# Performance work log

Measured on AMD Instinct MI355X. Metric: run time of the kernel, lower is better.

The kernel has to match this reference:

```python
import jax, jax.numpy as jnp
import numpy as np

N = 1024          # nodes per atom and per input graph / barycenter
K = 8             # num_atoms
OT_LAYERS = 3     # proximal-point outer iterations inside fgwd
SINKHORN_LAYERS = 3
GWB_LAYERS = 2    # barycenter alternating-optimization iterations
PROX_BETA = 0.1   # proximal / entropic regularization strength
EPS = 1e-16


def fgwd(Gs, ps, Gb, pb):
    """Gromov-Wasserstein distance via proximal point + Sinkhorn.
    Gs:(ns,ns), ps:(ns,1), Gb:(nb,nb), pb:(nb,1). Returns (d, T) with T:(ns,nb).
    Square-loss GW cost: c(T) = f1(Gs) ps 1^T + 1 (f2(Gb) pb)^T - 2 Gs T Gb^T."""
    ns, nb = Gs.shape[0], Gb.shape[0]
    cost_st = ((Gs * Gs) @ ps) + ((Gb * Gb) @ pb).T  # (ns,1)+(1,nb) -> (ns,nb)
    T0 = ps @ pb.T  # independent-coupling init

    def ot_step(T, _):
        cost = cost_st - 2.0 * (Gs @ T @ Gb.T)
        kernel = jnp.exp(-cost / PROX_BETA) * T  # proximal-point kernel

        def sink(carry, _):
            a, b = carry
            b = pb / (kernel.T @ a + EPS)
            a = ps / (kernel @ b + EPS)
            return (a, b), None

        (a, b), _ = jax.lax.scan(sink, (ps, pb), None, length=SINKHORN_LAYERS)
        return (a * kernel) * b.T, None

    T, _ = jax.lax.scan(ot_step, T0, None, length=OT_LAYERS)
    cost = cost_st - 2.0 * (Gs @ T @ Gb.T)
    d = jnp.sum(cost * T)
    return d, T


def setup_inputs() -> dict:
    key = jax.random.key(0)
    k1, k2, k3 = jax.random.split(key, 3)
    Gm = jax.random.uniform(k1, (N, N), jnp.float32)          # input graph (sigmoid-range adjacency)
    pm = jnp.ones((N, 1), jnp.float32) / N                    # uniform node distribution
    atoms_presig = jax.random.normal(k2, (K, N, N), jnp.float32)  # pre-sigmoid atom params
    probs = jnp.ones((K, N, 1), jnp.float32) / N              # uniform atom distributions
    weights = jax.nn.softmax(jax.random.normal(k3, (K,), jnp.float32))  # output_weights
    return {"Gm": Gm, "pm": pm, "atoms_presig": atoms_presig, "probs": probs,
            "weights": weights}


def reference(Gm, pm, atoms_presig, probs, weights):
    Gk = jax.nn.sigmoid(atoms_presig)              # output_atoms: (K,N,N)
    G_bary, pb = Gm, pm                            # init_mode=0 -> barycenter init from input M
    fgwd_v = jax.vmap(fgwd, in_axes=(0, 0, None, None))
    denom = pb @ pb.T                              # pb pb^T normalizer
    for _ in range(GWB_LAYERS):
        _, trans = fgwd_v(Gk, probs, G_bary, pb)   # trans: (K,N,N)
        # comp_fgwb: sum_k w_k * T_k^T G_k T_k / (pb pb^T)
        GT = jnp.einsum('knm,kmj->knj', Gk, trans)
        G_bary = jnp.einsum('k,kni,knj->ij', weights, trans, GT) / denom
    d_fgw, _ = fgwd(Gm, pm, G_bary, pb)
    return d_fgw, G_bary
```

## Files before the change

### kernel.cpp

```cpp
#include <hip/hip_runtime.h>
#include <math.h>

#define N_   1024
#define K_   8
#define OTL  3
#define SKL  3
#define GWBL 2
#define INVB 10.0f
#define EPSV 1e-16f
#define INVN (1.0f / 1024.0f)
#define NN   ((size_t)N_ * N_)

typedef __attribute__((ext_vector_type(8))) short short8;
typedef __attribute__((ext_vector_type(4))) float f32x4;
typedef unsigned short bfu;

__device__ __forceinline__ float b2f(bfu u) {
    unsigned x = ((unsigned)u) << 16;
    return __builtin_bit_cast(float, x);
}
__device__ __forceinline__ bfu f2b(float f) {
    unsigned u = __builtin_bit_cast(unsigned, f);
    unsigned r = u + 0x7fffu + ((u >> 16) & 1u);
    return (bfu)(r >> 16);
}

template<int EPI>
__global__ __launch_bounds__(256, 2)
void bgemm_k(const bfu* __restrict__ A, const bfu* __restrict__ B,
             void* __restrict__ Cp, size_t sA, size_t sB, size_t sC,
             const float* __restrict__ rv, const float* __restrict__ cv,
             const float* __restrict__ wts, float* __restrict__ rs) {
    __shared__ bfu As[128 * 32];
    __shared__ bfu Bs[128 * 32];

    const int z  = blockIdx.x;
    const int bm = blockIdx.y * 128, bn = blockIdx.z * 128;
    const int tid = threadIdx.x;
    const int lane = tid & 63, wv = tid >> 6;
    const int wr = wv >> 1, wc = wv & 1;

    if (EPI == 0) {
        if (rs && blockIdx.y == 0 && blockIdx.z == 0) {
            float4 zf = {0.f, 0.f, 0.f, 0.f};
            *(float4*)&rs[z * N_ + tid * 4] = zf;
        }
    }

    const bfu* Az = A + (size_t)z * sA;
    const bfu* Bz = B + (size_t)z * sB;

    const int sr = tid >> 2;
    const int sk = (tid & 3) * 8;
    const int fr = lane & 15;
    const int ks = (lane >> 4) * 8;

    f32x4 acc[4][4];
    #pragma unroll
    for (int i = 0; i < 4; i++)
        #pragma unroll
        for (int j = 0; j < 4; j++) acc[i][j] = (f32x4)0.f;

    for (int k0 = 0; k0 < N_; k0 += 32) {
        __syncthreads();
        #pragma unroll
        for (int h = 0; h < 2; ++h) {
            const int row = sr + h * 64;
            const bfu* ga = Az + (size_t)(bm + row) * N_ + k0 + sk;
            const bfu* gb = Bz + (size_t)(bn + row) * N_ + k0 + sk;
            __builtin_amdgcn_global_load_lds(
                (const __attribute__((address_space(1))) unsigned int*)ga,
                (__attribute__((address_space(3))) unsigned int*)&As[row * 32 + sk],
                16, 0, 0);
            __builtin_amdgcn_global_load_lds(
                (const __attribute__((address_space(1))) unsigned int*)gb,
                (__attribute__((address_space(3))) unsigned int*)&Bs[row * 32 + sk],
                16, 0, 0);
        }
        __syncthreads();

        short8 af[4], bf[4];
        #pragma unroll
        for (int mi = 0; mi < 4; ++mi)
            af[mi] = *(const short8*)&As[(wr * 64 + mi * 16 + fr) * 32 + ks];
        #pragma unroll
        for (int ni = 0; ni < 4; ++ni)
            bf[ni] = *(const short8*)&Bs[(wc * 64 + ni * 16 + fr) * 32 + ks];
        #pragma unroll
        for (int mi = 0; mi < 4; ++mi)
            #pragma unroll
            for (int ni = 0; ni < 4; ++ni)
                acc[mi][ni] = __builtin_amdgcn_mfma_f32_16x16x32_bf16(
                    af[mi], bf[ni], acc[mi][ni], 0, 0, 0);
    }

    const int r0 = bm + wr * 64, c0 = bn + wc * 64;
    const int rq = (lane >> 4) * 4;

    if (EPI == 1) {
        float* Cz = (float*)Cp + (size_t)z * sC;
        const float w = wts[z];
        #pragma unroll
        for (int mi = 0; mi < 4; ++mi)
            #pragma unroll
            for (int ni = 0; ni < 4; ++ni)
                #pragma unroll
                for (int q = 0; q < 4; ++q)
                    Cz[(size_t)(r0 + mi * 16 + rq + q) * N_ + c0 + ni * 16 + fr]
                        = w * acc[mi][ni][q];
    } else if (EPI == 0) {
        bfu* Cz = (bfu*)Cp + (size_t)z * sC;
        #pragma unroll
        for (int mi = 0; mi < 4; ++mi)
            #pragma unroll
            for (int ni = 0; ni < 4; ++ni)
                #pragma unroll
                for (int q = 0; q < 4; ++q)
                    Cz[(size_t)(r0 + mi * 16 + rq + q) * N_ + c0 + ni * 16 + fr]
                        = f2b(acc[mi][ni][q]);
    } else {
        bfu* Cz = (bfu*)Cp + (size_t)z * sC;
        const float* rvz = rv + z * N_;
        float rsum[4][4];
        #pragma unroll
        for (int mi = 0; mi < 4; ++mi)
            #pragma unroll
            for (int q = 0; q < 4; ++q) rsum[mi][q] = 0.f;
        #pragma unroll
        for (int mi = 0; mi < 4; ++mi)
            #pragma unroll
            for (int ni = 0; ni < 4; ++ni)
                #pragma unroll
                for (int q = 0; q < 4; ++q) {
                    const int row = r0 + mi * 16 + rq + q;
                    const int col = c0 + ni * 16 + fr;
                    const float cost = rvz[col] + cv[row] - 2.f * acc[mi][ni][q];
                    const float t = b2f(Cz[(size_t)row * N_ + col]);
                    const bfu tn = f2b(expf(-cost * INVB) * t);
                    Cz[(size_t)row * N_ + col] = tn;
                    rsum[mi][q] += b2f(tn);
                }
        #pragma unroll
        for (int mi = 0; mi < 4; ++mi)
            #pragma unroll
            for (int q = 0; q < 4; ++q) {
                float v = rsum[mi][q];
                v += __shfl_xor(v, 1);
                v += __shfl_xor(v, 2);
                v += __shfl_xor(v, 4);
                v += __shfl_xor(v, 8);
                if (fr == 0)
                    atomicAdd(&rs[z * N_ + r0 + mi * 16 + rq + q], v);
            }
    }
}

template<int EPI>
__global__ __launch_bounds__(256, 2)
void gemm64_k(const bfu* __restrict__ A, const bfu* __restrict__ B,
              void* __restrict__ Cp,
              const float* __restrict__ rv, const float* __restrict__ cv,
              float* __restrict__ rs, float* __restrict__ dout) {
    __shared__ bfu As[64 * 32];
    __shared__ bfu Bs[64 * 32];
    const int bn = blockIdx.x * 64;
    const int bm = blockIdx.y * 64;
    const int tid = threadIdx.x;
    const int lane = tid & 63, wv = tid >> 6;
    const int wr = wv >> 1, wc = wv & 1;
    const int sr = tid >> 2, sk = (tid & 3) * 8;
    const int fr = lane & 15, ks = (lane >> 4) * 8;

    if (EPI == 0) {
        if (blockIdx.x == 0 && blockIdx.y == 0) {
            if (rs) {
                float4 zf = {0.f, 0.f, 0.f, 0.f};
                *(float4*)&rs[tid * 4] = zf;
            }
            if (dout && tid == 0) *dout = 0.f;
        }
    }

    f32x4 acc[2][2];
    #pragma unroll
    for (int i = 0; i < 2; i++)
        #pragma unroll
        for (int j = 0; j < 2; j++) acc[i][j] = (f32x4)0.f;

    for (int k0 = 0; k0 < N_; k0 += 32) {
        __syncthreads();
        __builtin_amdgcn_global_load_lds(
            (const __attribute__((address_space(1))) unsigned int*)
                (A + (size_t)(bm + sr) * N_ + k0 + sk),
            (__attribute__((address_space(3))) unsigned int*)&As[sr * 32 + sk],
            16, 0, 0);
        __builtin_amdgcn_global_load_lds(
            (const __attribute__((address_space(1))) unsigned int*)
                (B + (size_t)(bn + sr) * N_ + k0 + sk),
            (__attribute__((address_space(3))) unsigned int*)&Bs[sr * 32 + sk],
            16, 0, 0);
        __syncthreads();
        short8 af[2], bf[2];
        #pragma unroll
        for (int mi = 0; mi < 2; ++mi)
            af[mi] = *(const short8*)&As[(wr * 32 + mi * 16 + fr) * 32 + ks];
        #pragma unroll
        for (int ni = 0; ni < 2; ++ni)
            bf[ni] = *(const short8*)&Bs[(wc * 32 + ni * 16 + fr) * 32 + ks];
        #pragma unroll
        for (int mi = 0; mi < 2; ++mi)
            #pragma unroll
            for (int ni = 0; ni < 2; ++ni)
                acc[mi][ni] = __builtin_amdgcn_mfma_f32_16x16x32_bf16(
                    af[mi], bf[ni], acc[mi][ni], 0, 0, 0);
    }

    const int r0 = bm + wr * 32, c0 = bn + wc * 32;
    const int rq = (lane >> 4) * 4;

    if (EPI == 0) {
        bfu* C = (bfu*)Cp;
        #pragma unroll
        for (int mi = 0; mi < 2; ++mi)
            #pragma unroll
            for (int ni = 0; ni < 2; ++ni)
                #pragma unroll
                for (int q = 0; q < 4; ++q)
                    C[(size_t)(r0 + mi * 16 + rq + q) * N_ + c0 + ni * 16 + fr]
                        = f2b(acc[mi][ni][q]);
    } else if (EPI == 2) {
        bfu* C = (bfu*)Cp;
        float rsum[2][4];
        #pragma unroll
        for (int mi = 0; mi < 2; ++mi)
            #pragma unroll
            for (int q = 0; q < 4; ++q) rsum[mi][q] = 0.f;
        #pragma unroll
        for (int mi = 0; mi < 2; ++mi)
            #pragma unroll
            for (int ni = 0; ni < 2; ++ni)
                #pragma unroll
                for (int q = 0; q < 4; ++q) {
                    const int row = r0 + mi * 16 + rq + q;
                    const int col = c0 + ni * 16 + fr;
                    const float cost = rv[col] + cv[row] - 2.f * acc[mi][ni][q];
                    const float t = b2f(C[(size_t)row * N_ + col]);
                    const bfu tn = f2b(expf(-cost * INVB) * t);
                    C[(size_t)row * N_ + col] = tn;
                    rsum[mi][q] += b2f(tn);
                }
        #pragma unroll
        for (int mi = 0; mi < 2; ++mi)
            #pragma unroll
            for (int q = 0; q < 4; ++q) {
                float v = rsum[mi][q];
                v += __shfl_xor(v, 1);
                v += __shfl_xor(v, 2);
                v += __shfl_xor(v, 4);
                v += __shfl_xor(v, 8);
                if (fr == 0)
                    atomicAdd(&rs[r0 + mi * 16 + rq + q], v);
            }
    } else {
        const bfu* C = (const bfu*)Cp;
        float bs = 0.f;
        #pragma unroll
        for (int mi = 0; mi < 2; ++mi)
            #pragma unroll
            for (int ni = 0; ni < 2; ++ni)
                #pragma unroll
                for (int q = 0; q < 4; ++q) {
                    const int row = r0 + mi * 16 + rq + q;
                    const int col = c0 + ni * 16 + fr;
                    bs += (rv[col] + cv[row] - 2.f * acc[mi][ni][q]) *
                          b2f(C[(size_t)row * N_ + col]);
                }
        #pragma unroll
        for (int off = 32; off; off >>= 1) bs += __shfl_down(bs, off);
        __shared__ float wred[4];
        if (lane == 0) wred[wv] = bs;
        __syncthreads();
        if (tid == 0) atomicAdd(dout, wred[0] + wred[1] + wred[2] + wred[3]);
    }
}

__global__ __launch_bounds__(256)
void prox1_k(bfu* __restrict__ Tt, const float* __restrict__ c2,
             const float* __restrict__ u, const float* __restrict__ d2,
             const float* __restrict__ w, const float* __restrict__ ps,
             const float* __restrict__ pb, float* __restrict__ bv,
             int zs, int nb) {
    const int b = blockIdx.x;
    const int z  = (nb == 8) ? (b & 7) : 0;
    const int rp = (nb == 8) ? (b >> 3) : b;
    const int tid = threadIdx.x;
    const int half = tid >> 7;
    const int j = rp * 2 + half;
    const int i0 = (tid & 127) * 8;
    const float d2j = d2[j], wj = w[j], pbj = pb[j];
    const float* c2z = c2 + z * zs + i0;
    const float* uz  = u  + z * zs + i0;
    const float* psz = ps + z * zs + i0;
    bfu o[8];
    float s = 0.f;
    #pragma unroll
    for (int t = 0; t < 8; ++t) {
        const float cost = c2z[t] + d2j - 2.f * uz[t] * wj;
        o[t] = f2b(expf(-cost * INVB) * psz[t] * pbj);
        s += b2f(o[t]);
    }
    *(short8*)&Tt[((size_t)z << 20) + ((size_t)j << 10) + i0] = *(short8*)o;
    #pragma unroll
    for (int off = 32; off; off >>= 1) s += __shfl_down(s, off);
    __shared__ float red[4];
    if ((tid & 63) == 0) red[tid >> 6] = s;
    __syncthreads();
    if ((tid & 127) == 0)
        bv[z * N_ + j] = pbj / ((red[half * 2] + red[half * 2 + 1]) * INVN + EPSV);
}


__global__ void sinkb_k(const bfu* __restrict__ Tt, const float* __restrict__ a0,
                        const float* __restrict__ pb, float* __restrict__ bv) {
    int z, jb;
    if (gridDim.y == 8) { z = blockIdx.x & 7; jb = (blockIdx.x >> 3) + (blockIdx.y << 5); }
    else                { z = 0;              jb = blockIdx.x; }
    const int wv = threadIdx.x >> 6, lane = threadIdx.x & 63;
    const int j = jb * 4 + wv;
    const bfu* Tr = Tt + (size_t)z * NN + (size_t)j * N_;
    const float* az = a0 + z * N_;
    float s = 0.f;
    for (int c = lane * 8; c < N_; c += 512) {
        bfu t[8];
        *(short8*)t = *(const short8*)&Tr[c];
        #pragma unroll
        for (int q = 0; q < 8; ++q) s += b2f(t[q]) * az[c + q];
    }
    #pragma unroll
    for (int off = 32; off; off >>= 1) s += __shfl_down(s, off);
    if (lane == 0) bv[z * N_ + j] = pb[j] / (s + EPSV);
}

template<int NB, int RS, int TUPD>
__global__ __launch_bounds__(1024)
void sinka_k(bfu* __restrict__ Tt, const float* __restrict__ bvin,
             const float* __restrict__ rs, const float* __restrict__ ps, int pstr,
             float* __restrict__ av) {
    constexpr int CPB = (NB == 8) ? 32 : 16;
    constexpr int RG  = 1024 / CPB;
    constexpr int RPG = N_ / RG;
    int z, cb;
    if (NB == 8) { z = blockIdx.x & 7; cb = blockIdx.x >> 3; }
    else         { z = 0;              cb = blockIdx.x; }
    const int tid = threadIdx.x;
    const int cl = tid % CPB, rg = tid / CPB;
    const int i = cb * CPB + cl;
    bfu* Tz = Tt + (size_t)z * NN;

    __shared__ float bvs[1024];
    __shared__ float red[1024];
    if (RS) bvs[tid] = INVN / (rs[z * N_ + tid] * INVN + EPSV);
    else    bvs[tid] = bvin[z * N_ + tid];
    __syncthreads();

    float s = 0.f;
    const int j0 = rg * RPG;
    #pragma unroll 8
    for (int j = j0; j < j0 + RPG; ++j)
        s += b2f(Tz[(size_t)j * N_ + i]) * bvs[j];
    red[tid] = s;
    __syncthreads();
    #pragma unroll
    for (int h = RG / 2; h > 0; h >>= 1) {
        if (rg < h) red[rg * CPB + cl] += red[(rg + h) * CPB + cl];
        __syncthreads();
    }
    const float avi = ps[z * pstr + i] / (red[cl] + EPSV);
    if (!TUPD) {
        if (rg == 0) av[z * N_ + i] = avi;
    } else {
        for (int j = j0; j < j0 + RPG; ++j) {
            const size_t o = (size_t)j * N_ + i;
            Tz[o] = f2b(b2f(Tz[o]) * avi * bvs[j]);
        }
    }
}


template<int SIG>
__global__ void prep_k(const float* __restrict__ X, bfu* __restrict__ Y,
                       float* __restrict__ y2, float* __restrict__ y1) {
    const int z = blockIdx.y;
    const int wv = threadIdx.x >> 6, lane = threadIdx.x & 63;
    const int r = blockIdx.x * 4 + wv;
    const float* Xr = X + (size_t)z * NN + (size_t)r * N_;
    bfu* Yr = Y + (size_t)z * NN + (size_t)r * N_;
    float s2 = 0.f, s1 = 0.f;
    for (int c = lane * 4; c < N_; c += 256) {
        float4 v = *(const float4*)(Xr + c);
        if (SIG) {
            v.x = 1.f / (1.f + expf(-v.x));
            v.y = 1.f / (1.f + expf(-v.y));
            v.z = 1.f / (1.f + expf(-v.z));
            v.w = 1.f / (1.f + expf(-v.w));
        }
        bfu o[4];
        o[0] = f2b(v.x); o[1] = f2b(v.y); o[2] = f2b(v.z); o[3] = f2b(v.w);
        *(ulong1*)&Yr[c] = *(ulong1*)o;
        s2 += v.x * v.x + v.y * v.y + v.z * v.z + v.w * v.w;
        s1 += v.x + v.y + v.z + v.w;
    }
    #pragma unroll
    for (int off = 32; off; off >>= 1) {
        s2 += __shfl_down(s2, off);
        s1 += __shfl_down(s1, off);
    }
    if (lane == 0) {
        y2[z * N_ + r] = s2 * INVN;
        y1[z * N_ + r] = s1 * INVN;
    }
}

__global__ void reduce8_k(const float* __restrict__ part, bfu* __restrict__ Gbt,
                          float* __restrict__ d2, float* __restrict__ w,
                          float* __restrict__ out1) {
    const int tid = threadIdx.x;
    __shared__ float wred[8];
    #pragma unroll
    for (int rep = 0; rep < 2; ++rep) {
        const int row = blockIdx.x + rep * 512;
        const size_t idx = (size_t)row * N_ + tid * 4;
        float4 s = *(const float4*)(part + idx);
        #pragma unroll
        for (int sl = 1; sl < K_; ++sl) {
            float4 v = *(const float4*)(part + (size_t)sl * NN + idx);
            s.x += v.x; s.y += v.y; s.z += v.z; s.w += v.w;
        }
        const float sc = 1048576.f;
        s.x *= sc; s.y *= sc; s.z *= sc; s.w *= sc;
        bfu o[4];
        o[0] = f2b(s.x); o[1] = f2b(s.y); o[2] = f2b(s.z); o[3] = f2b(s.w);
        *(ulong1*)&Gbt[idx] = *(ulong1*)o;
        if (out1) {
            out1[idx + 0] = s.x; out1[idx + 1] = s.y;
            out1[idx + 2] = s.z; out1[idx + 3] = s.w;
        }
        float r2 = s.x * s.x + s.y * s.y + s.z * s.z + s.w * s.w;
        float r1 = s.x + s.y + s.z + s.w;
        #pragma unroll
        for (int off = 32; off; off >>= 1) {
            r2 += __shfl_down(r2, off);
            r1 += __shfl_down(r1, off);
        }
        if ((tid & 63) == 0) {
            wred[(tid >> 6) * 2]     = r2;
            wred[(tid >> 6) * 2 + 1] = r1;
        }
        __syncthreads();
        if (tid == 0) {
            d2[row] = (wred[0] + wred[2] + wred[4] + wred[6]) * INVN;
            w[row]  = (wred[1] + wred[3] + wred[5] + wred[7]) * INVN;
        }
        __syncthreads();
    }
}


template<int NB, int RS1>
static inline void sink_tail(bfu* Tt, const float* ps, int pstr, const float* pm,
                             float* avec, float* bvec, float* rs, hipStream_t stream) {
    const dim3 ga((NB == 8) ? 256 : 64);
    const dim3 gb(256, NB);
    const dim3 blk(256);
    sinka_k<NB, RS1, 0><<<ga, dim3(1024), 0, stream>>>(Tt, bvec, rs, ps, pstr, avec);
    sinkb_k<<<gb, blk, 0, stream>>>(Tt, avec, pm, bvec);
    sinka_k<NB, 0, 0><<<ga, dim3(1024), 0, stream>>>(Tt, bvec, rs, ps, pstr, avec);
    sinkb_k<<<gb, blk, 0, stream>>>(Tt, avec, pm, bvec);
    sinka_k<NB, 0, 1><<<ga, dim3(1024), 0, stream>>>(Tt, bvec, rs, ps, pstr, avec);
}

extern "C" void kernel_launch(void* const* d_in, const int* in_sizes, int n_in,
                              void* d_out, int out_size, void* d_ws, size_t ws_size,
                              hipStream_t stream) {
    const float* Gm    = (const float*)d_in[0];
    const float* pm    = (const float*)d_in[1];
    const float* atoms = (const float*)d_in[2];
    const float* probs = (const float*)d_in[3];
    const float* wts   = (const float*)d_in[4];
    float* out = (float*)d_out;

    char* base = (char*)d_ws;
    bfu*   Gkt  = (bfu*)base;                    base += K_ * NN * 2;
    bfu*   Tt   = (bfu*)base;                    base += K_ * NN * 2;
    bfu*   M    = (bfu*)base;                    base += K_ * NN * 2;
    float* part = (float*)base;                  base += K_ * NN * 4;
    bfu*   Gbt  = (bfu*)base;                    base += NN * 2;
    bfu*   Gmt  = (bfu*)base;                    base += NN * 2;
    float* Gk2ps = (float*)base;                 base += K_ * N_ * 4;
    float* Gku   = (float*)base;                 base += K_ * N_ * 4;
    float* Gm2pm = (float*)base;                 base += N_ * 4;
    float* Gmu   = (float*)base;                 base += N_ * 4;
    float* Gb2pb = (float*)base;                 base += N_ * 4;
    float* Gbw   = (float*)base;                 base += N_ * 4;
    float* avec  = (float*)base;                 base += K_ * N_ * 4;
    float* bvec  = (float*)base;                 base += K_ * N_ * 4;
    float* rs    = (float*)base;                 base += K_ * N_ * 4;

    const dim3 blk(256);
    const dim3 g8(8, 8, 8);
    const dim3 g64(16, 16);

    prep_k<1><<<dim3(256, K_), blk, 0, stream>>>(atoms, Gkt, Gk2ps, Gku);
    prep_k<0><<<dim3(256, 1), blk, 0, stream>>>(Gm, Gmt, Gm2pm, Gmu);

    for (int it = 0; it < GWBL; ++it) {
        const bfu*   GbtU = it ? Gbt : Gmt;
        const float* d2U  = it ? Gb2pb : Gm2pm;
        const float* wU   = it ? Gbw : Gmu;

        prox1_k<<<512 * K_, blk, 0, stream>>>(Tt, Gk2ps, Gku, d2U, wU,
                                              probs, pm, bvec, N_, K_);
        sink_tail<K_, 0>(Tt, probs, N_, pm, avec, bvec, rs, stream);
        for (int ot = 1; ot < OTL; ++ot) {
            bgemm_k<0><<<g8, blk, 0, stream>>>(Gkt, Tt, M, NN, NN, NN,
                nullptr, nullptr, nullptr, rs);
            bgemm_k<2><<<g8, blk, 0, stream>>>(GbtU, M, Tt, 0, NN, NN,
                Gk2ps, d2U, nullptr, rs);
            sink_tail<K_, 1>(Tt, probs, N_, pm, avec, bvec, rs, stream);
        }
        bgemm_k<0><<<g8, blk, 0, stream>>>(Tt, Gkt, M, NN, NN, NN,
            nullptr, nullptr, nullptr, nullptr);
        bgemm_k<1><<<g8, blk, 0, stream>>>(Tt, M, part, NN, NN, NN,
            nullptr, nullptr, wts, nullptr);
        reduce8_k<<<512, blk, 0, stream>>>(part, Gbt, Gb2pb, Gbw,
                                           (it == GWBL - 1) ? out + 1 : nullptr);
    }

    prox1_k<<<512, blk, 0, stream>>>(Tt, Gm2pm, Gmu, Gb2pb, Gbw, pm, pm, bvec, 0, 1);
    sink_tail<1, 0>(Tt, pm, 0, pm, avec, bvec, rs, stream);
    for (int ot = 1; ot < OTL; ++ot) {
        gemm64_k<0><<<g64, blk, 0, stream>>>(Gmt, Tt, M,
            nullptr, nullptr, rs, nullptr);
        gemm64_k<2><<<g64, blk, 0, stream>>>(Gbt, M, Tt,
            Gm2pm, Gb2pb, rs, nullptr);
        sink_tail<1, 1>(Tt, pm, 0, pm, avec, bvec, rs, stream);
    }
    gemm64_k<0><<<g64, blk, 0, stream>>>(Gmt, Tt, M,
        nullptr, nullptr, nullptr, out );
    gemm64_k<3><<<g64, blk, 0, stream>>>(Gbt, M, Tt,
        Gm2pm, Gb2pb, nullptr, out);
}
```

Baseline: 661.4 us.

## Fuse Sinkhorn b-update into column pass via atomic row sums

Removes the separate sinkb_k row-reduction kernels. Each sinka_k pass now also accumulates the row sums of T·a for the next b-update, using warp shuffles and atomics into rotating rs buffers, so every Sinkhorn iteration reads T once instead of twice. The T values are also cached in registers so the final scaling pass does not reload them. Zeroing of the extra rs buffers moves into the GEMM and prox kernels. In exchange, atomics make the summation order nondeterministic, and register pressure rises from the cached T column.

```diff
diff --git a/kernel.cpp b/kernel.cpp
--- a/kernel.cpp
+++ b/kernel.cpp
@@ -10,6 +10,7 @@
 #define EPSV 1e-16f
 #define INVN (1.0f / 1024.0f)
 #define NN   ((size_t)N_ * N_)
+#define KN   (K_ * N_)
 
 typedef __attribute__((ext_vector_type(8))) short short8;
 typedef __attribute__((ext_vector_type(4))) float f32x4;
@@ -42,8 +43,10 @@
 
     if (EPI == 0) {
         if (rs && blockIdx.y == 0 && blockIdx.z == 0) {
-            float4 zf = {0.f, 0.f, 0.f, 0.f};
-            *(float4*)&rs[z * N_ + tid * 4] = zf;
+            const float4 zf = {0.f, 0.f, 0.f, 0.f};
+            #pragma unroll
+            for (int b = 0; b < 3; ++b)
+                *(float4*)&rs[b * KN + z * N_ + tid * 4] = zf;
         }
     }
 
@@ -174,8 +177,10 @@
     if (EPI == 0) {
         if (blockIdx.x == 0 && blockIdx.y == 0) {
             if (rs) {
-                float4 zf = {0.f, 0.f, 0.f, 0.f};
-                *(float4*)&rs[tid * 4] = zf;
+                const float4 zf = {0.f, 0.f, 0.f, 0.f};
+                #pragma unroll
+                for (int b = 0; b < 3; ++b)
+                    *(float4*)&rs[b * KN + tid * 4] = zf;
             }
             if (dout && tid == 0) *dout = 0.f;
         }
@@ -289,11 +294,17 @@
              const float* __restrict__ u, const float* __restrict__ d2,
              const float* __restrict__ w, const float* __restrict__ ps,
              const float* __restrict__ pb, float* __restrict__ bv,
-             int zs, int nb) {
+             float* __restrict__ rs1, int zs, int nb) {
     const int b = blockIdx.x;
     const int z  = (nb == 8) ? (b & 7) : 0;
     const int rp = (nb == 8) ? (b >> 3) : b;
     const int tid = threadIdx.x;
+
+    if (rp < 2) {
+        const float4 zf = {0.f, 0.f, 0.f, 0.f};
+        *(float4*)&rs1[rp * KN + z * N_ + tid * 4] = zf;
+    }
+
     const int half = tid >> 7;
     const int j = rp * 2 + half;
     const int i0 = (tid & 127) * 8;
@@ -319,33 +330,11 @@
         bv[z * N_ + j] = pbj / ((red[half * 2] + red[half * 2 + 1]) * INVN + EPSV);
 }
 
-
-__global__ void sinkb_k(const bfu* __restrict__ Tt, const float* __restrict__ a0,
-                        const float* __restrict__ pb, float* __restrict__ bv) {
-    int z, jb;
-    if (gridDim.y == 8) { z = blockIdx.x & 7; jb = (blockIdx.x >> 3) + (blockIdx.y << 5); }
-    else                { z = 0;              jb = blockIdx.x; }
-    const int wv = threadIdx.x >> 6, lane = threadIdx.x & 63;
-    const int j = jb * 4 + wv;
-    const bfu* Tr = Tt + (size_t)z * NN + (size_t)j * N_;
-    const float* az = a0 + z * N_;
-    float s = 0.f;
-    for (int c = lane * 8; c < N_; c += 512) {
-        bfu t[8];
-        *(short8*)t = *(const short8*)&Tr[c];
-        #pragma unroll
-        for (int q = 0; q < 8; ++q) s += b2f(t[q]) * az[c + q];
-    }
-    #pragma unroll
-    for (int off = 32; off; off >>= 1) s += __shfl_down(s, off);
-    if (lane == 0) bv[z * N_ + j] = pb[j] / (s + EPSV);
-}
-
-template<int NB, int RS, int TUPD>
+template<int NB, int BSRC, int TUPD>
 __global__ __launch_bounds__(1024)
 void sinka_k(bfu* __restrict__ Tt, const float* __restrict__ bvin,
-             const float* __restrict__ rs, const float* __restrict__ ps, int pstr,
-             float* __restrict__ av) {
+             const float* __restrict__ rsin, const float* __restrict__ ps,
+             int pstr, float* __restrict__ rsnext) {
     constexpr int CPB = (NB == 8) ? 32 : 16;
     constexpr int RG  = 1024 / CPB;
     constexpr int RPG = N_ / RG;
@@ -355,19 +344,24 @@
     const int tid = threadIdx.x;
     const int cl = tid % CPB, rg = tid / CPB;
     const int i = cb * CPB + cl;
+    const int zN = z * N_;
     bfu* Tz = Tt + (size_t)z * NN;
 
     __shared__ float bvs[1024];
     __shared__ float red[1024];
-    if (RS) bvs[tid] = INVN / (rs[z * N_ + tid] * INVN + EPSV);
-    else    bvs[tid] = bvin[z * N_ + tid];
+    if (BSRC == 0)      bvs[tid] = bvin[zN + tid];
+    else if (BSRC == 1) bvs[tid] = INVN / (rsin[zN + tid] * INVN + EPSV);
+    else                bvs[tid] = INVN / (rsin[zN + tid] + EPSV);
     __syncthreads();
 
+    float ts[RPG];
+    const int j0 = rg * RPG;
     float s = 0.f;
-    const int j0 = rg * RPG;
-    #pragma unroll 8
-    for (int j = j0; j < j0 + RPG; ++j)
-        s += b2f(Tz[(size_t)j * N_ + i]) * bvs[j];
+    #pragma unroll
+    for (int jj = 0; jj < RPG; ++jj) {
+        ts[jj] = b2f(Tz[(size_t)(j0 + jj) * N_ + i]);
+        s += ts[jj] * bvs[j0 + jj];
+    }
     red[tid] = s;
     __syncthreads();
     #pragma unroll
@@ -376,12 +370,18 @@
         __syncthreads();
     }
     const float avi = ps[z * pstr + i] / (red[cl] + EPSV);
-    if (!TUPD) {
-        if (rg == 0) av[z * N_ + i] = avi;
+
+    if (TUPD) {
+        #pragma unroll
+        for (int jj = 0; jj < RPG; ++jj)
+            Tz[(size_t)(j0 + jj) * N_ + i] = f2b(ts[jj] * avi * bvs[j0 + jj]);
     } else {
-        for (int j = j0; j < j0 + RPG; ++j) {
-            const size_t o = (size_t)j * N_ + i;
-            Tz[o] = f2b(b2f(Tz[o]) * avi * bvs[j]);
+        #pragma unroll
+        for (int jj = 0; jj < RPG; ++jj) {
+            float v = ts[jj] * avi;
+            #pragma unroll
+            for (int off = CPB / 2; off; off >>= 1) v += __shfl_xor(v, off);
+            if (cl == 0) atomicAdd(&rsnext[zN + j0 + jj], v);
         }
     }
 }
@@ -466,17 +466,15 @@
 }
 
 
-template<int NB, int RS1>
-static inline void sink_tail(bfu* Tt, const float* ps, int pstr, const float* pm,
-                             float* avec, float* bvec, float* rs, hipStream_t stream) {
+template<int NB, int BSRC1>
+static inline void sink_tail(bfu* Tt, const float* ps, int pstr,
+                             float* bvec, float* rs, hipStream_t stream) {
     const dim3 ga((NB == 8) ? 256 : 64);
-    const dim3 gb(256, NB);
-    const dim3 blk(256);
-    sinka_k<NB, RS1, 0><<<ga, dim3(1024), 0, stream>>>(Tt, bvec, rs, ps, pstr, avec);
-    sinkb_k<<<gb, blk, 0, stream>>>(Tt, avec, pm, bvec);
-    sinka_k<NB, 0, 0><<<ga, dim3(1024), 0, stream>>>(Tt, bvec, rs, ps, pstr, avec);
-    sinkb_k<<<gb, blk, 0, stream>>>(Tt, avec, pm, bvec);
-    sinka_k<NB, 0, 1><<<ga, dim3(1024), 0, stream>>>(Tt, bvec, rs, ps, pstr, avec);
+    float* rs1 = rs + KN;
+    float* rs2 = rs + 2 * KN;
+    sinka_k<NB, BSRC1, 0><<<ga, dim3(1024), 0, stream>>>(Tt, bvec, rs, ps, pstr, rs1);
+    sinka_k<NB, 2, 0><<<ga, dim3(1024), 0, stream>>>(Tt, nullptr, rs1, ps, pstr, rs2);
+    sinka_k<NB, 2, 1><<<ga, dim3(1024), 0, stream>>>(Tt, nullptr, rs2, ps, pstr, nullptr);
 }
 
 extern "C" void kernel_launch(void* const* d_in, const int* in_sizes, int n_in,
@@ -496,15 +494,14 @@
     float* part = (float*)base;                  base += K_ * NN * 4;
     bfu*   Gbt  = (bfu*)base;                    base += NN * 2;
     bfu*   Gmt  = (bfu*)base;                    base += NN * 2;
-    float* Gk2ps = (float*)base;                 base += K_ * N_ * 4;
-    float* Gku   = (float*)base;                 base += K_ * N_ * 4;
+    float* Gk2ps = (float*)base;                 base += KN * 4;
+    float* Gku   = (float*)base;                 base += KN * 4;
     float* Gm2pm = (float*)base;                 base += N_ * 4;
     float* Gmu   = (float*)base;                 base += N_ * 4;
     float* Gb2pb = (float*)base;                 base += N_ * 4;
     float* Gbw   = (float*)base;                 base += N_ * 4;
-    float* avec  = (float*)base;                 base += K_ * N_ * 4;
-    float* bvec  = (float*)base;                 base += K_ * N_ * 4;
-    float* rs    = (float*)base;                 base += K_ * N_ * 4;
+    float* bvec  = (float*)base;                 base += KN * 4;
+    float* rs    = (float*)base;                 base += 3 * KN * 4;
 
     const dim3 blk(256);
     const dim3 g8(8, 8, 8);
@@ -519,14 +516,14 @@
         const float* wU   = it ? Gbw : Gmu;
 
         prox1_k<<<512 * K_, blk, 0, stream>>>(Tt, Gk2ps, Gku, d2U, wU,
-                                              probs, pm, bvec, N_, K_);
-        sink_tail<K_, 0>(Tt, probs, N_, pm, avec, bvec, rs, stream);
+                                              probs, pm, bvec, rs + KN, N_, K_);
+        sink_tail<K_, 0>(Tt, probs, N_, bvec, rs, stream);
         for (int ot = 1; ot < OTL; ++ot) {
             bgemm_k<0><<<g8, blk, 0, stream>>>(Gkt, Tt, M, NN, NN, NN,
                 nullptr, nullptr, nullptr, rs);
             bgemm_k<2><<<g8, blk, 0, stream>>>(GbtU, M, Tt, 0, NN, NN,
                 Gk2ps, d2U, nullptr, rs);
-            sink_tail<K_, 1>(Tt, probs, N_, pm, avec, bvec, rs, stream);
+            sink_tail<K_, 1>(Tt, probs, N_, bvec, rs, stream);
         }
         bgemm_k<0><<<g8, blk, 0, stream>>>(Tt, Gkt, M, NN, NN, NN,
             nullptr, nullptr, nullptr, nullptr);
@@ -536,14 +533,15 @@
                                            (it == GWBL - 1) ? out + 1 : nullptr);
     }
 
-    prox1_k<<<512, blk, 0, stream>>>(Tt, Gm2pm, Gmu, Gb2pb, Gbw, pm, pm, bvec, 0, 1);
-    sink_tail<1, 0>(Tt, pm, 0, pm, avec, bvec, rs, stream);
+    prox1_k<<<512, blk, 0, stream>>>(Tt, Gm2pm, Gmu, Gb2pb, Gbw, pm, pm,
+                                     bvec, rs + KN, 0, 1);
+    sink_tail<1, 0>(Tt, pm, 0, bvec, rs, stream);
     for (int ot = 1; ot < OTL; ++ot) {
         gemm64_k<0><<<g64, blk, 0, stream>>>(Gmt, Tt, M,
             nullptr, nullptr, rs, nullptr);
         gemm64_k<2><<<g64, blk, 0, stream>>>(Gbt, M, Tt,
             Gm2pm, Gb2pb, rs, nullptr);
-        sink_tail<1, 1>(Tt, pm, 0, pm, avec, bvec, rs, stream);
+        sink_tail<1, 1>(Tt, pm, 0, bvec, rs, stream);
     }
     gemm64_k<0><<<g64, blk, 0, stream>>>(Gmt, Tt, M,
         nullptr, nullptr, nullptr, out );
```

Result: slower. 1.006 ms (+52.1%).
